# Kernel optimization log

Hardware: AMD Instinct MI355X
Metric: run time of the kernel (lower is better)

The kernel has to match this reference:

```python
import jax, jax.numpy as jnp
import numpy as np

NUM_NEURONS = 4_000_000
NUM_WEIGHTS = 8
SRC_SIZE = 2_000_000


def setup_inputs() -> dict:
    key = jax.random.key(0)
    k1, k2, k3, k4, k5, k6 = jax.random.split(key, 6)
    values_a = jax.random.normal(k1, (SRC_SIZE,), dtype=jnp.float32)
    values_b = jax.random.normal(k2, (SRC_SIZE,), dtype=jnp.float32)
    weights = jax.random.normal(k3, (NUM_WEIGHTS,), dtype=jnp.float32)
    idx_a = jax.random.randint(k4, (SRC_SIZE,), 0, SRC_SIZE, dtype=jnp.int64 if jax.config.jax_enable_x64 else jnp.int32).astype(jnp.int32)
    idx_b = jax.random.randint(k5, (SRC_SIZE,), 0, SRC_SIZE).astype(jnp.int32)
    concat_idx = jax.random.randint(k6, (NUM_NEURONS * NUM_WEIGHTS,), 0, 2 * SRC_SIZE).astype(jnp.int32)
    return {
        "values_a": values_a,
        "values_b": values_b,
        "weights": weights,
        "idx_a": idx_a,
        "idx_b": idx_b,
        "concat_idx": concat_idx,
    }


def reference(values_a, values_b, weights, idx_a, idx_b, concat_idx):
    # GatherModule stage 1: per-source-layer gather of needed ordinals, concatenated
    # in layer order.  [2*SRC_SIZE]
    layer_inputs_needed = jnp.concatenate([values_a[idx_a], values_b[idx_b]])
    # GatherModule stage 2: one entry per (neuron, input) pair.  [NUM_NEURONS*NUM_WEIGHTS]
    gathered = layer_inputs_needed[concat_idx]
    # WeightedRuleLayer: per-input-position weights shared across all neurons,
    # weighted sum over rule-body inputs + tanh activation.  [NUM_NEURONS]
    g = gathered.reshape(-1, weights.shape[0])
    return jnp.tanh(jnp.einsum("nk,k->n", g, weights))
```

## Files before the change

### kernel.cpp

```cpp
#include <hip/hip_runtime.h>
#include <hip/hip_fp16.h>

constexpr int SRC = 2000000;
constexpr int NN  = 4000000;
constexpr int TBL = 2 * SRC;
constexpr int HALF_TBL = TBL / 2;

typedef int v4i __attribute__((ext_vector_type(4)));

__global__ __launch_bounds__(256) void build_chunk(
    const float* __restrict__ v, const int* __restrict__ idx,
    __half* __restrict__ tout, int lo, int hi)
{
    const int stride = gridDim.x * blockDim.x;
    for (int i = blockIdx.x * blockDim.x + threadIdx.x; i < SRC; i += stride) {
        int c = __builtin_nontemporal_load(&idx[i]);
        if (c >= lo && c < hi) {
            tout[i] = __float2half_rn(v[c]);
        }
    }
}

template<int PHASE>
__global__ __launch_bounds__(256) void neuron_pass(
    const int*    __restrict__ cidx,
    const __half* __restrict__ table,
    const float*  __restrict__ w,
    float*        __restrict__ po)
{
    __shared__ float ws[8];
    if (threadIdx.x < 8) ws[threadIdx.x] = w[threadIdx.x];
    __syncthreads();
    const float w0 = ws[0], w1 = ws[1], w2 = ws[2], w3 = ws[3];
    const float w4 = ws[4], w5 = ws[5], w6 = ws[6], w7 = ws[7];

    const int stride = gridDim.x * blockDim.x;
    for (int n = blockIdx.x * blockDim.x + threadIdx.x; n < NN; n += stride) {
        const v4i* p = reinterpret_cast<const v4i*>(cidx) + (size_t)n * 2;
        v4i c0 = __builtin_nontemporal_load(p);
        v4i c1 = __builtin_nontemporal_load(p + 1);

        float acc;
        if (PHASE == 0) acc = 0.0f;
        else            acc = __builtin_nontemporal_load(&po[n]);

        #define TERM(c, wk)                                                  \
            if (PHASE == 0 ? ((c) < HALF_TBL) : ((c) >= HALF_TBL))           \
                acc += __half2float(table[(c)]) * (wk);
        TERM(c0.x, w0) TERM(c0.y, w1) TERM(c0.z, w2) TERM(c0.w, w3)
        TERM(c1.x, w4) TERM(c1.y, w5) TERM(c1.z, w6) TERM(c1.w, w7)
        #undef TERM

        if (PHASE == 0) __builtin_nontemporal_store(acc, &po[n]);
        else            __builtin_nontemporal_store(tanhf(acc), &po[n]);
    }
}

__global__ __launch_bounds__(256) void fused_kernel(
    const float* __restrict__ va, const float* __restrict__ vb,
    const int*   __restrict__ ia, const int*   __restrict__ ib,
    const int*   __restrict__ cidx,
    const float* __restrict__ w,
    float* __restrict__ out)
{
    __shared__ float ws[8];
    if (threadIdx.x < 8) ws[threadIdx.x] = w[threadIdx.x];
    __syncthreads();

    const int stride = gridDim.x * blockDim.x;
    for (int n = blockIdx.x * blockDim.x + threadIdx.x; n < NN; n += stride) {
        const int4* p = reinterpret_cast<const int4*>(cidx) + (size_t)n * 2;
        int4 c0 = p[0];
        int4 c1 = p[1];
        int c[8] = {c0.x, c0.y, c0.z, c0.w, c1.x, c1.y, c1.z, c1.w};
        float acc = 0.f;
        #pragma unroll
        for (int k = 0; k < 8; ++k) {
            int ci = c[k];
            float v = (ci < SRC) ? va[ia[ci]] : vb[ib[ci - SRC]];
            acc += v * ws[k];
        }
        out[n] = tanhf(acc);
    }
}

extern "C" void kernel_launch(void* const* d_in, const int* in_sizes, int n_in,
                              void* d_out, int out_size, void* d_ws, size_t ws_size,
                              hipStream_t stream) {
    const float* va   = (const float*)d_in[0];
    const float* vb   = (const float*)d_in[1];
    const float* w    = (const float*)d_in[2];
    const int*   ia   = (const int*)d_in[3];
    const int*   ib   = (const int*)d_in[4];
    const int*   cidx = (const int*)d_in[5];
    float* out = (float*)d_out;

    const size_t table_bytes = (size_t)TBL * sizeof(__half);
    if (ws_size >= table_bytes) {
        __half* table = (__half*)d_ws;
        const int HS = SRC / 2;
        build_chunk<<<2048, 256, 0, stream>>>(va, ia, table,        0,  HS);
        build_chunk<<<2048, 256, 0, stream>>>(va, ia, table,       HS, SRC);
        build_chunk<<<2048, 256, 0, stream>>>(vb, ib, table + SRC,  0,  HS);
        build_chunk<<<2048, 256, 0, stream>>>(vb, ib, table + SRC, HS, SRC);
        neuron_pass<0><<<2048, 256, 0, stream>>>(cidx, table, w, out);
        neuron_pass<1><<<2048, 256, 0, stream>>>(cidx, table, w, out);
    } else {
        fused_kernel<<<2048, 256, 0, stream>>>(va, vb, ia, ib, cidx, w, out);
    }
}
```

Before: 427.5 us.

## Fuse table build into one vectorized kernel and restructure neuron pass loads

Replaces four range-filtered table-build launches with a single kernel. Each thread handles 8 entries, using vector index loads and one packed 16-byte half store. This removes the repeated reads of idx across launches and the per-launch overhead, but gives up the cache locality that splitting the gather source range was meant to provide. The neuron pass now loads weights straight into registers instead of through shared memory, and it issues all eight conditional table loads before a single multiply-add chain, to improve memory-level parallelism.

```diff
diff --git a/kernel.cpp b/kernel.cpp
--- a/kernel.cpp
+++ b/kernel.cpp
@@ -8,16 +8,34 @@
 
 typedef int v4i __attribute__((ext_vector_type(4)));
 
-__global__ __launch_bounds__(256) void build_chunk(
-    const float* __restrict__ v, const int* __restrict__ idx,
-    __half* __restrict__ tout, int lo, int hi)
+__global__ __launch_bounds__(256) void build_all(
+    const float* __restrict__ va, const float* __restrict__ vb,
+    const int*   __restrict__ ia, const int*   __restrict__ ib,
+    __half* __restrict__ table)
 {
-    const int stride = gridDim.x * blockDim.x;
-    for (int i = blockIdx.x * blockDim.x + threadIdx.x; i < SRC; i += stride) {
-        int c = __builtin_nontemporal_load(&idx[i]);
-        if (c >= lo && c < hi) {
-            tout[i] = __float2half_rn(v[c]);
-        }
+    const int ngroups = TBL / 8;
+    const int agroups = SRC / 8;
+    const int stride  = gridDim.x * blockDim.x;
+    for (int i = blockIdx.x * blockDim.x + threadIdx.x; i < ngroups; i += stride) {
+        const float* v;
+        const int*   id;
+        int base;
+        if (i < agroups) { v = va; id = ia; base = i * 8; }
+        else             { v = vb; id = ib; base = (i - agroups) * 8; }
+        v4i ca = __builtin_nontemporal_load(reinterpret_cast<const v4i*>(id + base));
+        v4i cb = __builtin_nontemporal_load(reinterpret_cast<const v4i*>(id + base + 4));
+        float f0 = v[ca.x], f1 = v[ca.y], f2 = v[ca.z], f3 = v[ca.w];
+        float f4 = v[cb.x], f5 = v[cb.y], f6 = v[cb.z], f7 = v[cb.w];
+        uint4 o;
+        o.x = (unsigned)__half_as_ushort(__float2half_rn(f0))
+            | ((unsigned)__half_as_ushort(__float2half_rn(f1)) << 16);
+        o.y = (unsigned)__half_as_ushort(__float2half_rn(f2))
+            | ((unsigned)__half_as_ushort(__float2half_rn(f3)) << 16);
+        o.z = (unsigned)__half_as_ushort(__float2half_rn(f4))
+            | ((unsigned)__half_as_ushort(__float2half_rn(f5)) << 16);
+        o.w = (unsigned)__half_as_ushort(__float2half_rn(f6))
+            | ((unsigned)__half_as_ushort(__float2half_rn(f7)) << 16);
+        reinterpret_cast<uint4*>(table)[i] = o;
     }
 }
 
@@ -28,28 +46,42 @@
     const float*  __restrict__ w,
     float*        __restrict__ po)
 {
-    __shared__ float ws[8];
-    if (threadIdx.x < 8) ws[threadIdx.x] = w[threadIdx.x];
-    __syncthreads();
-    const float w0 = ws[0], w1 = ws[1], w2 = ws[2], w3 = ws[3];
-    const float w4 = ws[4], w5 = ws[5], w6 = ws[6], w7 = ws[7];
+    float wk[8];
+    #pragma unroll
+    for (int k = 0; k < 8; ++k) wk[k] = w[k];
 
     const int stride = gridDim.x * blockDim.x;
     for (int n = blockIdx.x * blockDim.x + threadIdx.x; n < NN; n += stride) {
         const v4i* p = reinterpret_cast<const v4i*>(cidx) + (size_t)n * 2;
         v4i c0 = __builtin_nontemporal_load(p);
         v4i c1 = __builtin_nontemporal_load(p + 1);
+        float prev = (PHASE == 0) ? 0.0f : __builtin_nontemporal_load(&po[n]);
 
-        float acc;
-        if (PHASE == 0) acc = 0.0f;
-        else            acc = __builtin_nontemporal_load(&po[n]);
+        float v0 = 0.f, v1 = 0.f, v2 = 0.f, v3 = 0.f;
+        float v4_ = 0.f, v5 = 0.f, v6 = 0.f, v7 = 0.f;
+        if (PHASE == 0) {
+            if (c0.x <  HALF_TBL) v0  = __half2float(table[c0.x]);
+            if (c0.y <  HALF_TBL) v1  = __half2float(table[c0.y]);
+            if (c0.z <  HALF_TBL) v2  = __half2float(table[c0.z]);
+            if (c0.w <  HALF_TBL) v3  = __half2float(table[c0.w]);
+            if (c1.x <  HALF_TBL) v4_ = __half2float(table[c1.x]);
+            if (c1.y <  HALF_TBL) v5  = __half2float(table[c1.y]);
+            if (c1.z <  HALF_TBL) v6  = __half2float(table[c1.z]);
+            if (c1.w <  HALF_TBL) v7  = __half2float(table[c1.w]);
+        } else {
+            if (c0.x >= HALF_TBL) v0  = __half2float(table[c0.x]);
+            if (c0.y >= HALF_TBL) v1  = __half2float(table[c0.y]);
+            if (c0.z >= HALF_TBL) v2  = __half2float(table[c0.z]);
+            if (c0.w >= HALF_TBL) v3  = __half2float(table[c0.w]);
+            if (c1.x >= HALF_TBL) v4_ = __half2float(table[c1.x]);
+            if (c1.y >= HALF_TBL) v5  = __half2float(table[c1.y]);
+            if (c1.z >= HALF_TBL) v6  = __half2float(table[c1.z]);
+            if (c1.w >= HALF_TBL) v7  = __half2float(table[c1.w]);
+        }
 
-        #define TERM(c, wk)                                                  \
-            if (PHASE == 0 ? ((c) < HALF_TBL) : ((c) >= HALF_TBL))           \
-                acc += __half2float(table[(c)]) * (wk);
-        TERM(c0.x, w0) TERM(c0.y, w1) TERM(c0.z, w2) TERM(c0.w, w3)
-        TERM(c1.x, w4) TERM(c1.y, w5) TERM(c1.z, w6) TERM(c1.w, w7)
-        #undef TERM
+        float acc = prev
+                  + v0  * wk[0] + v1 * wk[1] + v2 * wk[2] + v3 * wk[3]
+                  + v4_ * wk[4] + v5 * wk[5] + v6 * wk[6] + v7 * wk[7];
 
         if (PHASE == 0) __builtin_nontemporal_store(acc, &po[n]);
         else            __builtin_nontemporal_store(tanhf(acc), &po[n]);
@@ -98,11 +130,7 @@
     const size_t table_bytes = (size_t)TBL * sizeof(__half);
     if (ws_size >= table_bytes) {
         __half* table = (__half*)d_ws;
-        const int HS = SRC / 2;
-        build_chunk<<<2048, 256, 0, stream>>>(va, ia, table,        0,  HS);
-        build_chunk<<<2048, 256, 0, stream>>>(va, ia, table,       HS, SRC);
-        build_chunk<<<2048, 256, 0, stream>>>(vb, ib, table + SRC,  0,  HS);
-        build_chunk<<<2048, 256, 0, stream>>>(vb, ib, table + SRC, HS, SRC);
+        build_all<<<2048, 256, 0, stream>>>(va, vb, ia, ib, table);
         neuron_pass<0><<<2048, 256, 0, stream>>>(cidx, table, w, out);
         neuron_pass<1><<<2048, 256, 0, stream>>>(cidx, table, w, out);
     } else {
```

Measured after the change: 424.6 us. About the same (-0.7%).

## Vectorize table build into two kernels and batch neuron-pass gathers

Applied to the files above, without the earlier changes.

Collapses the four range-split table-build launches into one launch per source layer. Each thread now handles 16 entries, using vector index loads and packed 128-bit half stores, which removes the repeated index re-reads and the per-element conditional stores. The neuron passes process two neurons per thread. Branchy conditional gathers become predicated loads that clamp to a dummy index with zero weight, so all 16 table loads can be in flight at once, at the cost of extra loads for entries outside the current half.

```diff
diff --git a/kernel.cpp b/kernel.cpp
--- a/kernel.cpp
+++ b/kernel.cpp
@@ -8,16 +8,29 @@
 
 typedef int v4i __attribute__((ext_vector_type(4)));
 
-__global__ __launch_bounds__(256) void build_chunk(
+__global__ __launch_bounds__(256) void build_half(
     const float* __restrict__ v, const int* __restrict__ idx,
-    __half* __restrict__ tout, int lo, int hi)
+    __half* __restrict__ tout)
 {
+    const int groups = SRC / 16;
     const int stride = gridDim.x * blockDim.x;
-    for (int i = blockIdx.x * blockDim.x + threadIdx.x; i < SRC; i += stride) {
-        int c = __builtin_nontemporal_load(&idx[i]);
-        if (c >= lo && c < hi) {
-            tout[i] = __float2half_rn(v[c]);
-        }
+    for (int i = blockIdx.x * blockDim.x + threadIdx.x; i < groups; i += stride) {
+        const int base = i * 16;
+        v4i c0 = __builtin_nontemporal_load(reinterpret_cast<const v4i*>(idx + base));
+        v4i c1 = __builtin_nontemporal_load(reinterpret_cast<const v4i*>(idx + base + 4));
+        v4i c2 = __builtin_nontemporal_load(reinterpret_cast<const v4i*>(idx + base + 8));
+        v4i c3 = __builtin_nontemporal_load(reinterpret_cast<const v4i*>(idx + base + 12));
+        float f0 = v[c0.x], f1 = v[c0.y], f2 = v[c0.z], f3 = v[c0.w];
+        float f4 = v[c1.x], f5 = v[c1.y], f6 = v[c1.z], f7 = v[c1.w];
+        float f8 = v[c2.x], f9 = v[c2.y], fa = v[c2.z], fb = v[c2.w];
+        float fc = v[c3.x], fd = v[c3.y], fe = v[c3.z], ff = v[c3.w];
+        #define PK(lo, hi) ((unsigned)__half_as_ushort(__float2half_rn(lo)) \
+                          | ((unsigned)__half_as_ushort(__float2half_rn(hi)) << 16))
+        uint4 o0 = { PK(f0, f1), PK(f2, f3), PK(f4, f5), PK(f6, f7) };
+        uint4 o1 = { PK(f8, f9), PK(fa, fb), PK(fc, fd), PK(fe, ff) };
+        #undef PK
+        reinterpret_cast<uint4*>(tout + base)[0] = o0;
+        reinterpret_cast<uint4*>(tout + base)[1] = o1;
     }
 }
 
@@ -28,31 +41,64 @@
     const float*  __restrict__ w,
     float*        __restrict__ po)
 {
-    __shared__ float ws[8];
-    if (threadIdx.x < 8) ws[threadIdx.x] = w[threadIdx.x];
-    __syncthreads();
-    const float w0 = ws[0], w1 = ws[1], w2 = ws[2], w3 = ws[3];
-    const float w4 = ws[4], w5 = ws[5], w6 = ws[6], w7 = ws[7];
+    float wk[8];
+    #pragma unroll
+    for (int k = 0; k < 8; ++k) wk[k] = w[k];
 
+    const int tid    = blockIdx.x * blockDim.x + threadIdx.x;
     const int stride = gridDim.x * blockDim.x;
-    for (int n = blockIdx.x * blockDim.x + threadIdx.x; n < NN; n += stride) {
-        const v4i* p = reinterpret_cast<const v4i*>(cidx) + (size_t)n * 2;
-        v4i c0 = __builtin_nontemporal_load(p);
-        v4i c1 = __builtin_nontemporal_load(p + 1);
 
-        float acc;
-        if (PHASE == 0) acc = 0.0f;
-        else            acc = __builtin_nontemporal_load(&po[n]);
+    for (int n = tid; n < NN; n += 2 * stride) {
+        const int n2   = n + stride;
+        const bool has2 = (n2 < NN);
+        const int m2   = has2 ? n2 : n;
 
-        #define TERM(c, wk)                                                  \
-            if (PHASE == 0 ? ((c) < HALF_TBL) : ((c) >= HALF_TBL))           \
-                acc += __half2float(table[(c)]) * (wk);
-        TERM(c0.x, w0) TERM(c0.y, w1) TERM(c0.z, w2) TERM(c0.w, w3)
-        TERM(c1.x, w4) TERM(c1.y, w5) TERM(c1.z, w6) TERM(c1.w, w7)
-        #undef TERM
+        const v4i* pa = reinterpret_cast<const v4i*>(cidx) + (size_t)n  * 2;
+        const v4i* pb = reinterpret_cast<const v4i*>(cidx) + (size_t)m2 * 2;
+        v4i a0 = __builtin_nontemporal_load(pa);
+        v4i a1 = __builtin_nontemporal_load(pa + 1);
+        v4i b0 = __builtin_nontemporal_load(pb);
+        v4i b1 = __builtin_nontemporal_load(pb + 1);
 
-        if (PHASE == 0) __builtin_nontemporal_store(acc, &po[n]);
-        else            __builtin_nontemporal_store(tanhf(acc), &po[n]);
+        #define SEL(c, k, cc, ww)                                            \
+            const bool p_##cc = (PHASE == 0) ? ((c) < HALF_TBL)              \
+                                             : ((c) >= HALF_TBL);            \
+            const int   cc = p_##cc ? (c) : (PHASE == 0 ? 0 : HALF_TBL);     \
+            const float ww = p_##cc ? wk[k] : 0.0f;
+        SEL(a0.x, 0, ca0, wa0) SEL(a0.y, 1, ca1, wa1)
+        SEL(a0.z, 2, ca2, wa2) SEL(a0.w, 3, ca3, wa3)
+        SEL(a1.x, 4, ca4, wa4) SEL(a1.y, 5, ca5, wa5)
+        SEL(a1.z, 6, ca6, wa6) SEL(a1.w, 7, ca7, wa7)
+        SEL(b0.x, 0, cb0, wb0) SEL(b0.y, 1, cb1, wb1)
+        SEL(b0.z, 2, cb2, wb2) SEL(b0.w, 3, cb3, wb3)
+        SEL(b1.x, 4, cb4, wb4) SEL(b1.y, 5, cb5, wb5)
+        SEL(b1.z, 6, cb6, wb6) SEL(b1.w, 7, cb7, wb7)
+        #undef SEL
+
+        const __half ga0 = table[ca0], ga1 = table[ca1], ga2 = table[ca2], ga3 = table[ca3];
+        const __half ga4 = table[ca4], ga5 = table[ca5], ga6 = table[ca6], ga7 = table[ca7];
+        const __half gb0 = table[cb0], gb1 = table[cb1], gb2 = table[cb2], gb3 = table[cb3];
+        const __half gb4 = table[cb4], gb5 = table[cb5], gb6 = table[cb6], gb7 = table[cb7];
+
+        float accA = (PHASE == 0) ? 0.0f : __builtin_nontemporal_load(&po[n]);
+        float accB = (PHASE == 0) ? 0.0f : __builtin_nontemporal_load(&po[m2]);
+
+        accA += __half2float(ga0) * wa0 + __half2float(ga1) * wa1
+              + __half2float(ga2) * wa2 + __half2float(ga3) * wa3
+              + __half2float(ga4) * wa4 + __half2float(ga5) * wa5
+              + __half2float(ga6) * wa6 + __half2float(ga7) * wa7;
+        accB += __half2float(gb0) * wb0 + __half2float(gb1) * wb1
+              + __half2float(gb2) * wb2 + __half2float(gb3) * wb3
+              + __half2float(gb4) * wb4 + __half2float(gb5) * wb5
+              + __half2float(gb6) * wb6 + __half2float(gb7) * wb7;
+
+        if (PHASE == 0) {
+            __builtin_nontemporal_store(accA, &po[n]);
+            if (has2) __builtin_nontemporal_store(accB, &po[n2]);
+        } else {
+            __builtin_nontemporal_store(tanhf(accA), &po[n]);
+            if (has2) __builtin_nontemporal_store(tanhf(accB), &po[n2]);
+        }
     }
 }
 
@@ -98,11 +144,8 @@
     const size_t table_bytes = (size_t)TBL * sizeof(__half);
     if (ws_size >= table_bytes) {
         __half* table = (__half*)d_ws;
-        const int HS = SRC / 2;
-        build_chunk<<<2048, 256, 0, stream>>>(va, ia, table,        0,  HS);
-        build_chunk<<<2048, 256, 0, stream>>>(va, ia, table,       HS, SRC);
-        build_chunk<<<2048, 256, 0, stream>>>(vb, ib, table + SRC,  0,  HS);
-        build_chunk<<<2048, 256, 0, stream>>>(vb, ib, table + SRC, HS, SRC);
+        build_half<<<512, 256, 0, stream>>>(va, ia, table);
+        build_half<<<512, 256, 0, stream>>>(vb, ib, table + SRC);
         neuron_pass<0><<<2048, 256, 0, stream>>>(cidx, table, w, out);
         neuron_pass<1><<<2048, 256, 0, stream>>>(cidx, table, w, out);
     } else {
```

Result: no change. 427.4 us (-0.0%).
